# Optimization experiments

Hardware: AMD Instinct MI355X
Metric: run time of the kernel (lower is better)

Reference implementation:

```python
import jax, jax.numpy as jnp
import numpy as np

H = W = 32          # gussin() is hard-coded to width=32 in BASE
C = 512             # BASE inner_nc; down conv is 1024->512
V = 1.5             # gaussian sigma


def _gaussian_weights():
    # Vectorized equivalent of gussin(1.5): g[p, x, y] for p = i*W + k,
    # g = exp(-((x-i)^2+(y-k)^2)/(2 v^2)) / (2 pi v^2), normalized per p.
    idx = np.arange(H, dtype=np.float64)
    d1 = (idx[:, None] - idx[None, :]) ** 2            # (i, x)
    d2 = d1[:, None, :, None] + d1[None, :, None, :]    # (i, k, x, y)
    g = np.exp(-d2 / (2.0 * V * V)) / (2.0 * np.pi * V * V)
    g = g.reshape(H * W, H, W)
    g = g / g.sum(axis=(1, 2), keepdims=True)
    return jnp.asarray(g, dtype=jnp.float32)


def _instance_norm(x, eps=1e-5):
    # InstanceNorm2d(affine=False): per-(b,c) mean/biased-var over (h,w)
    mu = x.mean(axis=(2, 3), keepdims=True)
    var = jnp.mean((x - mu) ** 2, axis=(2, 3), keepdims=True)
    return (x - mu) / jnp.sqrt(var + eps)


def _patches3(fm):
    # fm: (C, H+2, W+2) zero-padded map -> 3x3 patches: (H*W, C, 3, 3)
    p = jnp.stack([fm[:, di:di + H, dj:dj + W]
                   for di in range(3) for dj in range(3)], axis=-1)  # (C,H,W,9)
    return p.transpose(1, 2, 0, 3).reshape(H * W, C, 3, 3)


def setup_inputs() -> dict:
    key = jax.random.key(0)
    ks = jax.random.split(key, 4)
    x = jax.random.normal(ks[0], (1, C, H, W), jnp.float32)
    w_se1 = jax.random.normal(ks[1], (C // 16, C), jnp.float32) * 0.05   # SE squeeze fc
    w_se2 = jax.random.normal(ks[2], (C, C // 16), jnp.float32) * 0.05   # SE excite fc
    w_down = jax.random.normal(ks[3], (C, 2 * C, 1, 1), jnp.float32) * 0.05  # 1x1 conv 1024->512
    return {"x": x, "w_se1": w_se1, "w_se2": w_se2, "w_down": w_down}


def reference(x, w_se1, w_se2, w_down):
    gus = _gaussian_weights()                                # (HW, H, W), constant
    # --- SELayer(512, 16) ---
    s = x.mean(axis=(2, 3))                                  # (1, C) global avg pool
    s = jax.nn.relu(s @ w_se1.T)                             # (1, C/16)
    s = jax.nn.sigmoid(s @ w_se2.T)                          # (1, C)
    out32 = x * s[:, :, None, None]                          # (1, C, H, W)
    # --- gaussian-weighted pooling (einsum instead of (HW,C,H,W) broadcast) ---
    gus_out = jnp.einsum('pxy,cxy->pc', gus, out32[0])       # (HW, C)
    gus_out = gus_out.reshape(1, C, H, W)                    # raw reshape, as in torch .view
    # --- patch-based contextual self-attention (CSA) ---
    sig = jax.nn.sigmoid(out32)                              # (1, C, H, W)
    sig_pad = jnp.pad(sig[0], ((0, 0), (1, 1), (1, 1)))
    raw_pad = jnp.pad(out32[0], ((0, 0), (1, 1), (1, 1)))
    p_sig = _patches3(sig_pad)                               # (HW, C, 3, 3)
    p_raw = _patches3(raw_pad)                               # (HW, C, 3, 3)
    center = sig[0].transpose(1, 2, 0).reshape(H * W, C, 1, 1)  # center sigmoid vec per loc
    score = jnp.mean(center * p_sig, axis=1)                 # (HW, 3, 3)
    attn = jax.nn.softmax(score.reshape(H * W, 9), axis=1).reshape(H * W, 1, 3, 3)
    out_csa = jnp.sum(attn * p_raw, axis=(2, 3))             # (HW, C)
    out_csa = out_csa.reshape(1, C, H, W)                    # raw reshape, as in torch .view
    # --- concat + 1x1 conv down + InstanceNorm + LeakyReLU(0.2) ---
    cat = jnp.concatenate([gus_out, out_csa], axis=1)        # (1, 2C, H, W)
    y = jnp.einsum('bihw,oi->bohw', cat, w_down[:, :, 0, 0])
    y = _instance_norm(y)
    return jnp.where(y >= 0, y, 0.2 * y)
```

## Files before the change

kernel.cpp:

```cpp
#include <hip/hip_runtime.h>


typedef short short8 __attribute__((ext_vector_type(8)));
typedef short short4v __attribute__((ext_vector_type(4)));
typedef float floatx4 __attribute__((ext_vector_type(4)));
typedef float floatx16 __attribute__((ext_vector_type(16)));

__device__ __forceinline__ unsigned short f2bf(float x) {
  union { float f; unsigned u; } v; v.f = x;
  unsigned u = v.u;
  u = (u + 0x7fffu + ((u >> 16) & 1u)) >> 16;
  return (unsigned short)u;
}

__device__ __forceinline__ float block_reduce_256(float v, float* sm4) {
  #pragma unroll
  for (int off = 32; off >= 1; off >>= 1) v += __shfl_down(v, off);
  __syncthreads();
  if ((threadIdx.x & 63) == 0) sm4[threadIdx.x >> 6] = v;
  __syncthreads();
  return sm4[0] + sm4[1] + sm4[2] + sm4[3];
}

__device__ __forceinline__ void gauss_lds(float* g, int tid) {
  int ga = tid >> 3, gb0 = (tid & 7) * 4;
  float e[4]; float gs = 0.0f;
  #pragma unroll
  for (int q = 0; q < 4; q++) {
    float d = (float)(ga - (gb0 + q));
    e[q] = __expf(d * d * (-1.0f / 4.5f));
    gs += e[q];
  }
  gs += __shfl_xor(gs, 1, 8);
  gs += __shfl_xor(gs, 2, 8);
  gs += __shfl_xor(gs, 4, 8);
  float ginv = 1.0f / gs;
  #pragma unroll
  for (int q = 0; q < 4; q++) g[ga * 32 + gb0 + q] = e[q] * ginv;
}

__global__ void k_mean_cvt(const float* __restrict__ x, float* __restrict__ smean,
                           const float* __restrict__ wdn, unsigned short* __restrict__ Abf) {
  if (blockIdx.x >= 512) {
    int base = (blockIdx.x - 512) * 2048 + threadIdx.x * 8;
    float4 a = *(const float4*)&wdn[base];
    float4 b = *(const float4*)&wdn[base + 4];
    short8 s;
    s[0] = (short)f2bf(a.x); s[1] = (short)f2bf(a.y); s[2] = (short)f2bf(a.z); s[3] = (short)f2bf(a.w);
    s[4] = (short)f2bf(b.x); s[5] = (short)f2bf(b.y); s[6] = (short)f2bf(b.z); s[7] = (short)f2bf(b.w);
    *(short8*)&Abf[base] = s;
    return;
  }
  __shared__ float sm4[4];
  int c = blockIdx.x;
  const float* row = x + c * 1024;
  float s = 0.0f;
  for (int i = threadIdx.x; i < 1024; i += 256) s += row[i];
  float t = block_reduce_256(s, sm4);
  if (threadIdx.x == 0) smean[c] = t * (1.0f / 1024.0f);
}

__global__ void k_apply(const float* __restrict__ x, const float* __restrict__ smean,
                        const float* __restrict__ w1, const float* __restrict__ w2,
                        float* __restrict__ out32, float* __restrict__ out32T,
                        float* __restrict__ sigT) {
  __shared__ float sm[512];
  __shared__ float s1[32];
  __shared__ float sc[32];
  __shared__ float tile[32][33];
  int tid = threadIdx.x;
  for (int i = tid; i < 512; i += 256) sm[i] = smean[i];
  __syncthreads();
  int j = tid >> 3, l8 = tid & 7;
  float a = 0.0f;
  for (int cc = l8; cc < 512; cc += 8) a += sm[cc] * w1[j * 512 + cc];
  a += __shfl_down(a, 4, 8);
  a += __shfl_down(a, 2, 8);
  a += __shfl_down(a, 1, 8);
  if (l8 == 0) s1[j] = fmaxf(a, 0.0f);
  __syncthreads();
  int c0 = blockIdx.y * 32, hw0 = blockIdx.x * 32;
  if (tid < 32) {
    float bb = 0.0f;
    #pragma unroll
    for (int jj = 0; jj < 32; jj++) bb += s1[jj] * w2[(c0 + tid) * 32 + jj];
    sc[tid] = 1.0f / (1.0f + __expf(-bb));
  }
  __syncthreads();
  int tx = tid & 31, ty = tid >> 5;
  #pragma unroll
  for (int r = 0; r < 4; r++) {
    int c = ty + 8 * r;
    float v = x[(c0 + c) * 1024 + hw0 + tx] * sc[c];
    out32[(c0 + c) * 1024 + hw0 + tx] = v;
    tile[c][tx] = v;
  }
  __syncthreads();
  #pragma unroll
  for (int r = 0; r < 4; r++) {
    int hw = hw0 + ty + 8 * r;
    float v = tile[tx][ty + 8 * r];
    out32T[hw * 512 + c0 + tx] = v;
    sigT[hw * 512 + c0 + tx] = 1.0f / (1.0f + __expf(-v));
  }
}

__global__ void k_gausscsa(const float* __restrict__ out32, const float* __restrict__ sigT,
                           const float* __restrict__ out32T, unsigned short* __restrict__ catT) {
  if (blockIdx.x < 512) {
    __shared__ float g[1024];
    __shared__ float row[32 * 33];
    __shared__ float T[32 * 33];
    int c = blockIdx.x;
    int tid = threadIdx.x;
    gauss_lds(g, tid);
    for (int idx = tid; idx < 1024; idx += 256)
      row[(idx >> 5) * 33 + (idx & 31)] = out32[c * 1024 + idx];
    __syncthreads();
    {
      int xx = tid & 31, kg = tid >> 5;
      const float* g0 = g + kg * 128;
      const float* rw = row + xx * 33;
      float s0 = 0, s1 = 0, s2 = 0, s3 = 0;
      #pragma unroll 8
      for (int y = 0; y < 32; y++) {
        float vv = rw[y];
        s0 += g0[y] * vv;
        s1 += g0[32 + y] * vv;
        s2 += g0[64 + y] * vv;
        s3 += g0[96 + y] * vv;
      }
      int k0 = kg * 4;
      T[(k0 + 0) * 33 + xx] = s0;
      T[(k0 + 1) * 33 + xx] = s1;
      T[(k0 + 2) * 33 + xx] = s2;
      T[(k0 + 3) * 33 + xx] = s3;
    }
    __syncthreads();
    {
      int i = tid >> 3;
      int sub = tid & 7;
      int par = sub & 1, kq = sub >> 1;
      int kb = kq * 8 + par;
      const float* gi = g + i * 32;
      float s0 = 0, s1 = 0, s2 = 0, s3 = 0;
      #pragma unroll 8
      for (int xx = 0; xx < 32; xx++) {
        float gv = gi[xx];
        s0 += gv * T[(kb + 0) * 33 + xx];
        s1 += gv * T[(kb + 2) * 33 + xx];
        s2 += gv * T[(kb + 4) * 33 + xx];
        s3 += gv * T[(kb + 6) * 33 + xx];
      }
      short4v o;
      o[0] = (short)f2bf(s0); o[1] = (short)f2bf(s1);
      o[2] = (short)f2bf(s2); o[3] = (short)f2bf(s3);
      *(short4v*)&catT[(par * 512 + c) * 1024 + i * 16 + kq * 4] = o;
    }
  } else {
    int wv = threadIdx.x >> 6;
    int lane = threadIdx.x & 63;
    int p = (blockIdx.x - 512) * 4 + wv;
    int h = p >> 5, w = p & 31;
    int c0 = lane * 8;
    float4 ce0 = *(const float4*)&sigT[p * 512 + c0];
    float4 ce1 = *(const float4*)&sigT[p * 512 + c0 + 4];
    int qoff[9];
    float s[9];
    #pragma unroll
    for (int dd = 0; dd < 9; dd++) {
      int hh = h + dd / 3 - 1, ww = w + (dd % 3) - 1;
      bool v = (hh >= 0) && (hh < 32) && (ww >= 0) && (ww < 32);
      qoff[dd] = v ? (hh * 32 + ww) * 512 : -1;
      float a = 0.0f;
      if (v) {
        float4 n0 = *(const float4*)&sigT[qoff[dd] + c0];
        float4 n1 = *(const float4*)&sigT[qoff[dd] + c0 + 4];
        a = ce0.x * n0.x + ce0.y * n0.y + ce0.z * n0.z + ce0.w * n0.w
          + ce1.x * n1.x + ce1.y * n1.y + ce1.z * n1.z + ce1.w * n1.w;
      }
      #pragma unroll
      for (int off = 32; off >= 1; off >>= 1) a += __shfl_xor(a, off);
      s[dd] = a;
    }
    float mx = -1e30f;
    #pragma unroll
    for (int dd = 0; dd < 9; dd++) { s[dd] *= (1.0f / 512.0f); mx = fmaxf(mx, s[dd]); }
    float tot = 0.0f;
    #pragma unroll
    for (int dd = 0; dd < 9; dd++) { s[dd] = __expf(s[dd] - mx); tot += s[dd]; }
    float inv = 1.0f / tot;
    float o[8] = {0, 0, 0, 0, 0, 0, 0, 0};
    #pragma unroll
    for (int dd = 0; dd < 9; dd++) {
      if (qoff[dd] >= 0) {
        float att = s[dd] * inv;
        float4 r0 = *(const float4*)&out32T[qoff[dd] + c0];
        float4 r1 = *(const float4*)&out32T[qoff[dd] + c0 + 4];
        o[0] += att * r0.x; o[1] += att * r0.y; o[2] += att * r0.z; o[3] += att * r0.w;
        o[4] += att * r1.x; o[5] += att * r1.y; o[6] += att * r1.z; o[7] += att * r1.w;
      }
    }
    int kcol = 512 + (p >> 1);
    int nbase = (p & 1) * 512 + c0;
    #pragma unroll
    for (int q = 0; q < 8; q++) catT[(nbase + q) * 1024 + kcol] = f2bf(o[q]);
  }
}

__global__ void k_gemm(const unsigned short* __restrict__ Abf,
                       const unsigned short* __restrict__ Bbf,
                       float* __restrict__ y) {
  __shared__ float red[2][1024];
  int tid = threadIdx.x;
  int wv = tid >> 6, lane = tid & 63;
  int nt = wv & 1, kz = wv >> 1;
  int bm = (blockIdx.x >> 4) * 32;
  int nn = (blockIdx.x & 15) * 64 + nt * 32;
  int l32 = lane & 31, half = lane >> 5;
  const short8* ap = (const short8*)(Abf + (bm + l32) * 1024 + kz * 512 + half * 8);
  const short8* bp = (const short8*)(Bbf + (nn + l32) * 1024 + kz * 512 + half * 8);
  floatx16 acc = {};
  #pragma unroll 8
  for (int ks = 0; ks < 32; ks++) {
    short8 a = ap[ks * 2];
    short8 b = bp[ks * 2];
    acc = __builtin_amdgcn_mfma_f32_32x32x16_bf16(a, b, acc, 0, 0, 0);
  }
  if (kz == 1) {
    #pragma unroll
    for (int r = 0; r < 16; r++) red[nt][lane * 16 + r] = acc[r];
  }
  __syncthreads();
  if (kz == 0) {
    #pragma unroll
    for (int r = 0; r < 16; r++) {
      float v = acc[r] + red[nt][lane * 16 + r];
      int rowm = (r & 3) + 8 * (r >> 2) + 4 * half;
      y[(bm + rowm) * 1024 + nn + l32] = v;
    }
  }
}

__global__ void k_inorm(const float* __restrict__ y, float* __restrict__ out) {
  __shared__ float sm4[4];
  __shared__ float vrow[1024];
  int o = blockIdx.x;
  const float* r0 = y + o * 1024;
  float s = 0.0f, q = 0.0f;
  for (int i = threadIdx.x; i < 1024; i += 256) {
    float v = r0[i];
    vrow[i] = v;
    s += v; q += v * v;
  }
  float ts = block_reduce_256(s, sm4);
  float tq = block_reduce_256(q, sm4);
  float mean = ts * (1.0f / 1024.0f);
  float var = tq * (1.0f / 1024.0f) - mean * mean;
  float inv = rsqrtf(var + 1e-5f);
  for (int i = threadIdx.x; i < 1024; i += 256) {
    float v = (vrow[i] - mean) * inv;
    out[o * 1024 + i] = v >= 0.0f ? v : 0.2f * v;
  }
}

extern "C" void kernel_launch(void* const* d_in, const int* in_sizes, int n_in,
                              void* d_out, int out_size, void* d_ws, size_t ws_size,
                              hipStream_t stream) {
  const float* x      = (const float*)d_in[0];
  const float* w_se1  = (const float*)d_in[1];
  const float* w_se2  = (const float*)d_in[2];
  const float* w_down = (const float*)d_in[3];
  float* out = (float*)d_out;

  float* ws = (float*)d_ws;
  float* smean  = ws;
  float* out32  = ws + 1024;
  float* out32T = ws + 525312;
  float* sigT   = ws + 1049600;
  unsigned short* catT = (unsigned short*)(ws + 1573888);
  unsigned short* Abf  = (unsigned short*)(ws + 2098176);
  float* ybuf   = ws + 2360320;

  k_mean_cvt<<<768, 256, 0, stream>>>(x, smean, w_down, Abf);
  k_apply<<<dim3(32, 16), 256, 0, stream>>>(x, smean, w_se1, w_se2, out32, out32T, sigT);
  k_gausscsa<<<768, 256, 0, stream>>>(out32, sigT, out32T, catT);
  k_gemm<<<256, 256, 0, stream>>>(Abf, catT, ybuf);
  k_inorm<<<512, 256, 0, stream>>>(ybuf, out);
}
```

Baseline: 102.8 us.

## Vectorize loads across kernels and split GEMM K four ways over 512 blocks

The mean, instance-norm and gaussian-pooling stages now load and store with float4 in place of scalar accesses, and the LDS row stride is padded to 36 so vector reads stay aligned. The GEMM drops its two-way N split per block for a four-way K split over a single 32x32 tile per block, doubling the grid to 512 blocks and reducing three partial accumulators through LDS. These changes aim to cut instruction count and raise occupancy for the GEMM. The cost is a larger LDS reduction buffer and less A/B reuse within each block, and the stride-36 layout may bring back LDS bank conflicts on the transposed writes.

```diff
diff --git a/kernel.cpp b/kernel.cpp
--- a/kernel.cpp
+++ b/kernel.cpp
@@ -11,6 +11,10 @@
   unsigned u = v.u;
   u = (u + 0x7fffu + ((u >> 16) & 1u)) >> 16;
   return (unsigned short)u;
+}
+
+__device__ __forceinline__ float dot4(float4 a, float4 b) {
+  return a.x * b.x + a.y * b.y + a.z * b.z + a.w * b.w;
 }
 
 __device__ __forceinline__ float block_reduce_256(float v, float* sm4) {
@@ -53,9 +57,9 @@
   }
   __shared__ float sm4[4];
   int c = blockIdx.x;
-  const float* row = x + c * 1024;
-  float s = 0.0f;
-  for (int i = threadIdx.x; i < 1024; i += 256) s += row[i];
+  const float4* row = (const float4*)(x + c * 1024);
+  float4 v = row[threadIdx.x];
+  float s = v.x + v.y + v.z + v.w;
   float t = block_reduce_256(s, sm4);
   if (threadIdx.x == 0) smean[c] = t * (1.0f / 1024.0f);
 }
@@ -109,32 +113,34 @@
                            const float* __restrict__ out32T, unsigned short* __restrict__ catT) {
   if (blockIdx.x < 512) {
     __shared__ float g[1024];
-    __shared__ float row[32 * 33];
-    __shared__ float T[32 * 33];
+    __shared__ float row[32 * 36];
+    __shared__ float T[32 * 36];
     int c = blockIdx.x;
     int tid = threadIdx.x;
     gauss_lds(g, tid);
-    for (int idx = tid; idx < 1024; idx += 256)
-      row[(idx >> 5) * 33 + (idx & 31)] = out32[c * 1024 + idx];
+    {
+      int xx = tid >> 3, y4 = tid & 7;
+      float4 v = *(const float4*)&out32[c * 1024 + xx * 32 + y4 * 4];
+      *(float4*)&row[xx * 36 + y4 * 4] = v;
+    }
     __syncthreads();
     {
       int xx = tid & 31, kg = tid >> 5;
-      const float* g0 = g + kg * 128;
-      const float* rw = row + xx * 33;
+      int k0 = kg * 4;
+      const float4* rw4 = (const float4*)(row + xx * 36);
       float s0 = 0, s1 = 0, s2 = 0, s3 = 0;
-      #pragma unroll 8
-      for (int y = 0; y < 32; y++) {
-        float vv = rw[y];
-        s0 += g0[y] * vv;
-        s1 += g0[32 + y] * vv;
-        s2 += g0[64 + y] * vv;
-        s3 += g0[96 + y] * vv;
-      }
-      int k0 = kg * 4;
-      T[(k0 + 0) * 33 + xx] = s0;
-      T[(k0 + 1) * 33 + xx] = s1;
-      T[(k0 + 2) * 33 + xx] = s2;
-      T[(k0 + 3) * 33 + xx] = s3;
+      #pragma unroll
+      for (int y4 = 0; y4 < 8; y4++) {
+        float4 rv = rw4[y4];
+        s0 += dot4(*(const float4*)&g[(k0 + 0) * 32 + y4 * 4], rv);
+        s1 += dot4(*(const float4*)&g[(k0 + 1) * 32 + y4 * 4], rv);
+        s2 += dot4(*(const float4*)&g[(k0 + 2) * 32 + y4 * 4], rv);
+        s3 += dot4(*(const float4*)&g[(k0 + 3) * 32 + y4 * 4], rv);
+      }
+      T[(k0 + 0) * 36 + xx] = s0;
+      T[(k0 + 1) * 36 + xx] = s1;
+      T[(k0 + 2) * 36 + xx] = s2;
+      T[(k0 + 3) * 36 + xx] = s3;
     }
     __syncthreads();
     {
@@ -142,15 +148,14 @@
       int sub = tid & 7;
       int par = sub & 1, kq = sub >> 1;
       int kb = kq * 8 + par;
-      const float* gi = g + i * 32;
       float s0 = 0, s1 = 0, s2 = 0, s3 = 0;
-      #pragma unroll 8
-      for (int xx = 0; xx < 32; xx++) {
-        float gv = gi[xx];
-        s0 += gv * T[(kb + 0) * 33 + xx];
-        s1 += gv * T[(kb + 2) * 33 + xx];
-        s2 += gv * T[(kb + 4) * 33 + xx];
-        s3 += gv * T[(kb + 6) * 33 + xx];
+      #pragma unroll
+      for (int x4 = 0; x4 < 8; x4++) {
+        float4 gv = *(const float4*)&g[i * 32 + x4 * 4];
+        s0 += dot4(gv, *(const float4*)&T[(kb + 0) * 36 + x4 * 4]);
+        s1 += dot4(gv, *(const float4*)&T[(kb + 2) * 36 + x4 * 4]);
+        s2 += dot4(gv, *(const float4*)&T[(kb + 4) * 36 + x4 * 4]);
+        s3 += dot4(gv, *(const float4*)&T[(kb + 6) * 36 + x4 * 4]);
       }
       short4v o;
       o[0] = (short)f2bf(s0); o[1] = (short)f2bf(s1);
@@ -176,8 +181,7 @@
       if (v) {
         float4 n0 = *(const float4*)&sigT[qoff[dd] + c0];
         float4 n1 = *(const float4*)&sigT[qoff[dd] + c0 + 4];
-        a = ce0.x * n0.x + ce0.y * n0.y + ce0.z * n0.z + ce0.w * n0.w
-          + ce1.x * n1.x + ce1.y * n1.y + ce1.z * n1.z + ce1.w * n1.w;
+        a = dot4(ce0, n0) + dot4(ce1, n1);
       }
       #pragma unroll
       for (int off = 32; off >= 1; off >>= 1) a += __shfl_xor(a, off);
@@ -211,31 +215,33 @@
 __global__ void k_gemm(const unsigned short* __restrict__ Abf,
                        const unsigned short* __restrict__ Bbf,
                        float* __restrict__ y) {
-  __shared__ float red[2][1024];
+  __shared__ float red[3][1024];
   int tid = threadIdx.x;
   int wv = tid >> 6, lane = tid & 63;
-  int nt = wv & 1, kz = wv >> 1;
-  int bm = (blockIdx.x >> 4) * 32;
-  int nn = (blockIdx.x & 15) * 64 + nt * 32;
+  int bm = (blockIdx.x >> 5) * 32;
+  int nn = (blockIdx.x & 31) * 32;
   int l32 = lane & 31, half = lane >> 5;
-  const short8* ap = (const short8*)(Abf + (bm + l32) * 1024 + kz * 512 + half * 8);
-  const short8* bp = (const short8*)(Bbf + (nn + l32) * 1024 + kz * 512 + half * 8);
+  const short8* ap = (const short8*)(Abf + (bm + l32) * 1024 + wv * 256 + half * 8);
+  const short8* bp = (const short8*)(Bbf + (nn + l32) * 1024 + wv * 256 + half * 8);
   floatx16 acc = {};
-  #pragma unroll 8
-  for (int ks = 0; ks < 32; ks++) {
+  #pragma unroll
+  for (int ks = 0; ks < 16; ks++) {
     short8 a = ap[ks * 2];
     short8 b = bp[ks * 2];
     acc = __builtin_amdgcn_mfma_f32_32x32x16_bf16(a, b, acc, 0, 0, 0);
   }
-  if (kz == 1) {
-    #pragma unroll
-    for (int r = 0; r < 16; r++) red[nt][lane * 16 + r] = acc[r];
-  }
-  __syncthreads();
-  if (kz == 0) {
+  if (wv != 0) {
+    #pragma unroll
+    for (int r4 = 0; r4 < 4; r4++) {
+      float4 v = make_float4(acc[r4 * 4], acc[r4 * 4 + 1], acc[r4 * 4 + 2], acc[r4 * 4 + 3]);
+      *(float4*)&red[wv - 1][lane * 16 + r4 * 4] = v;
+    }
+  }
+  __syncthreads();
+  if (wv == 0) {
     #pragma unroll
     for (int r = 0; r < 16; r++) {
-      float v = acc[r] + red[nt][lane * 16 + r];
+      float v = acc[r] + red[0][lane * 16 + r] + red[1][lane * 16 + r] + red[2][lane * 16 + r];
       int rowm = (r & 3) + 8 * (r >> 2) + 4 * half;
       y[(bm + rowm) * 1024 + nn + l32] = v;
     }
@@ -246,22 +252,23 @@
   __shared__ float sm4[4];
   __shared__ float vrow[1024];
   int o = blockIdx.x;
-  const float* r0 = y + o * 1024;
-  float s = 0.0f, q = 0.0f;
-  for (int i = threadIdx.x; i < 1024; i += 256) {
-    float v = r0[i];
-    vrow[i] = v;
-    s += v; q += v * v;
-  }
+  int tid = threadIdx.x;
+  float4 v4 = *(const float4*)&y[o * 1024 + tid * 4];
+  *(float4*)&vrow[tid * 4] = v4;
+  float s = v4.x + v4.y + v4.z + v4.w;
+  float q = v4.x * v4.x + v4.y * v4.y + v4.z * v4.z + v4.w * v4.w;
   float ts = block_reduce_256(s, sm4);
   float tq = block_reduce_256(q, sm4);
   float mean = ts * (1.0f / 1024.0f);
   float var = tq * (1.0f / 1024.0f) - mean * mean;
   float inv = rsqrtf(var + 1e-5f);
-  for (int i = threadIdx.x; i < 1024; i += 256) {
-    float v = (vrow[i] - mean) * inv;
-    out[o * 1024 + i] = v >= 0.0f ? v : 0.2f * v;
-  }
+  float4 w4 = *(const float4*)&vrow[tid * 4];
+  float4 r4;
+  float a0 = (w4.x - mean) * inv; r4.x = a0 >= 0.0f ? a0 : 0.2f * a0;
+  float a1 = (w4.y - mean) * inv; r4.y = a1 >= 0.0f ? a1 : 0.2f * a1;
+  float a2 = (w4.z - mean) * inv; r4.z = a2 >= 0.0f ? a2 : 0.2f * a2;
+  float a3 = (w4.w - mean) * inv; r4.w = a3 >= 0.0f ? a3 : 0.2f * a3;
+  *(float4*)&out[o * 1024 + tid * 4] = r4;
 }
 
 extern "C" void kernel_launch(void* const* d_in, const int* in_sizes, int n_in,
@@ -285,6 +292,6 @@
   k_mean_cvt<<<768, 256, 0, stream>>>(x, smean, w_down, Abf);
   k_apply<<<dim3(32, 16), 256, 0, stream>>>(x, smean, w_se1, w_se2, out32, out32T, sigT);
   k_gausscsa<<<768, 256, 0, stream>>>(out32, sigT, out32T, catT);
-  k_gemm<<<256, 256, 0, stream>>>(Abf, catT, ybuf);
+  k_gemm<<<512, 256, 0, stream>>>(Abf, catT, ybuf);
   k_inorm<<<512, 256, 0, stream>>>(ybuf, out);
 }
```

Measured after the change: 100.3 us. 2.4% less time.
